# Kernel tuning notes

Hardware: AMD Instinct MI355X
Metric: run time of the kernel (lower is better)

## Reference

```python
import jax, jax.numpy as jnp
import numpy as np

N = 100000
D_IN = 256
C = 4          # num_classes
D_C = 32       # output_dim // num_classes
E = 1600000    # nnz per class adjacency


def setup_inputs() -> dict:
    key = jax.random.key(0)
    k1, k2, k3, k4, k5 = jax.random.split(key, 5)
    x = jax.random.normal(k1, (N, D_IN), dtype=jnp.float32)
    # kernel (input_dim, output_dim) split along axis=1 into C chunks -> [D_IN, C, D_C]
    W = jax.random.normal(k2, (D_IN, C, D_C), dtype=jnp.float32) * (2.0 / D_IN) ** 0.5
    rows = jax.random.randint(k3, (C, E), 0, N, dtype=jnp.int64)
    cols = jax.random.randint(k4, (C, E), 0, N, dtype=jnp.int64)
    vals = jax.random.uniform(k5, (C, E), dtype=jnp.float32)
    return {"x": x, "W": W, "rows": rows, "cols": cols, "vals": vals}


def reference(x, W, rows, cols, vals):
    # dropout with rate 0.0 is identity.
    n = x.shape[0]
    # per-class dense transform: tmp[:, c, :] = x @ W[:, c, :]
    tmp = jnp.einsum('nd,dcf->ncf', x, W)  # [N, C, D_C]

    def prop(r, c, v, t):
        # t: [N, D_C] features for one class; SpMM A_c @ t via gather+segment_sum
        msg = t[c] * v[:, None]                              # [E, D_C]
        return jax.ops.segment_sum(msg, r, num_segments=n)   # [N, D_C]

    out = jax.vmap(prop, in_axes=(0, 0, 0, 1))(rows, cols, vals, tmp)  # [C, N, D_C]
    z = jnp.transpose(out, (1, 0, 2)).reshape(n, -1)  # concat along feature axis -> [N, C*D_C]
    return jax.nn.relu(z)
```

## Files before the change

### kernel.cpp

```cpp
#include <hip/hip_runtime.h>
#include <hip/hip_bf16.h>
#include <hip/hip_fp16.h>

#define D_IN 256
#define D_OUT 128
#define D_C 32
#define NUM_C 4
#define RB_LOG 10
#define RB 1024
#define MB_MAX 400

typedef _Float16 f16x8 __attribute__((ext_vector_type(8)));
typedef float    f32x4 __attribute__((ext_vector_type(4)));

__global__ void wcvt_kernel(const float* __restrict__ W, __half* __restrict__ Wt) {
    int t = blockIdx.x * 256 + threadIdx.x;
    if (t >= D_IN * D_OUT) return;
    int col = t >> 8;
    int k   = t & 255;
    Wt[col * D_IN + k] = __float2half(W[k * D_OUT + col]);
}

__global__ __launch_bounds__(256) void gemm_kernel(const float* __restrict__ x,
                                                   const __half* __restrict__ Wt,
                                                   __half* __restrict__ tmp,
                                                   int Nrows) {
    __shared__ f16x8 As[2048];
    const int t    = threadIdx.x;
    const int brow = blockIdx.x * 64;

    const int w   = t >> 6;
    const int l   = t & 63;
    const int l15 = l & 15;
    const int hi  = l >> 4;

    f16x8 bf[8][2];
    #pragma unroll
    for (int ks = 0; ks < 8; ++ks)
        #pragma unroll
        for (int cti = 0; cti < 2; ++cti)
            bf[ks][cti] = *reinterpret_cast<const f16x8*>(
                Wt + (size_t)((w * 2 + cti) * 16 + l15) * D_IN + ks * 32 + hi * 8);

    #pragma unroll
    for (int i = 0; i < 8; ++i) {
        int ci  = i * 256 + t;
        int row = ci >> 5;
        int kc  = ci & 31;
        int grow = brow + row;
        float4 a0 = make_float4(0.f, 0.f, 0.f, 0.f);
        float4 a1 = make_float4(0.f, 0.f, 0.f, 0.f);
        if (grow < Nrows) {
            const float* src = x + (size_t)grow * D_IN + kc * 8;
            a0 = *reinterpret_cast<const float4*>(src);
            a1 = *reinterpret_cast<const float4*>(src + 4);
        }
        f16x8 h;
        h[0] = (_Float16)a0.x; h[1] = (_Float16)a0.y;
        h[2] = (_Float16)a0.z; h[3] = (_Float16)a0.w;
        h[4] = (_Float16)a1.x; h[5] = (_Float16)a1.y;
        h[6] = (_Float16)a1.z; h[7] = (_Float16)a1.w;
        As[kc * 64 + (row ^ kc)] = h;
    }
    __syncthreads();

    f32x4 acc[4][2] = {};

    #pragma unroll
    for (int rt = 0; rt < 4; ++rt) {
        const int arow = rt * 16 + l15;
        #pragma unroll
        for (int ks = 0; ks < 8; ++ks) {
            const int kcA = ks * 4 + hi;
            f16x8 afrag = As[kcA * 64 + (arow ^ kcA)];
            acc[rt][0] = __builtin_amdgcn_mfma_f32_16x16x32_f16(afrag, bf[ks][0], acc[rt][0], 0, 0, 0);
            acc[rt][1] = __builtin_amdgcn_mfma_f32_16x16x32_f16(afrag, bf[ks][1], acc[rt][1], 0, 0, 0);
        }
    }

    #pragma unroll
    for (int rt = 0; rt < 4; ++rt) {
        #pragma unroll
        for (int cti = 0; cti < 2; ++cti) {
            const int cio = cti * 16 + l15;
            #pragma unroll
            for (int r = 0; r < 4; ++r) {
                int grow = brow + rt * 16 + hi * 4 + r;
                if (grow < Nrows)
                    tmp[((size_t)w * Nrows + grow) * 32 + cio] = __float2half((float)acc[rt][cti][r]);
            }
        }
    }
}

__global__ __launch_bounds__(256) void bucket_hist_kernel(const int* __restrict__ rows,
                                                          int* __restrict__ bcnt,
                                                          int CE, int E, int NB, int MB) {
    __shared__ int h[MB_MAX];
    for (int i = threadIdx.x; i < MB; i += 256) h[i] = 0;
    __syncthreads();
    const int CE4 = CE >> 2;
    const int4* rows4 = reinterpret_cast<const int4*>(rows);
    int base4 = blockIdx.x * 4096;
    #pragma unroll 4
    for (int i = 0; i < 16; ++i) {
        int i4 = base4 + threadIdx.x + i * 256;
        if (i4 < CE4) {
            int e0 = i4 << 2;
            int c = (e0 >= 3 * E) ? 3 : (e0 >= 2 * E) ? 2 : (e0 >= E) ? 1 : 0;
            int4 rv = rows4[i4];
            atomicAdd(&h[c * NB + (rv.x >> RB_LOG)], 1);
            atomicAdd(&h[c * NB + (rv.y >> RB_LOG)], 1);
            atomicAdd(&h[c * NB + (rv.z >> RB_LOG)], 1);
            atomicAdd(&h[c * NB + (rv.w >> RB_LOG)], 1);
        }
    }
    if (blockIdx.x == 0 && threadIdx.x < (CE & 3)) {
        int e = (CE4 << 2) + threadIdx.x;
        int c = (e >= 3 * E) ? 3 : (e >= 2 * E) ? 2 : (e >= E) ? 1 : 0;
        atomicAdd(&h[c * NB + (rows[e] >> RB_LOG)], 1);
    }
    __syncthreads();
    for (int i = threadIdx.x; i < MB; i += 256)
        if (h[i]) atomicAdd(&bcnt[i], h[i]);
}

__global__ __launch_bounds__(512) void bucket_scan_kernel(const int* __restrict__ bcnt,
                                                          int* __restrict__ bstartP,
                                                          int* __restrict__ bheadLine,
                                                          int* __restrict__ bstartD,
                                                          int* __restrict__ starts,
                                                          int MB, int M, int slackLines) {
    __shared__ int sd[512];
    int t = threadIdx.x;
    int v = (t < MB) ? bcnt[t] : 0;
    int capL = ((v + 7) >> 3) + slackLines;
    sd[t] = capL; __syncthreads();
    for (int off = 1; off < 512; off <<= 1) {
        int add = (t >= off) ? sd[t - off] : 0;
        __syncthreads();
        sd[t] += add;
        __syncthreads();
    }
    int exclL = sd[t] - capL;
    if (t < MB) { bstartP[t] = exclL * 8; bheadLine[t] = exclL; }
    __syncthreads();
    sd[t] = v; __syncthreads();
    for (int off = 1; off < 512; off <<= 1) {
        int add = (t >= off) ? sd[t - off] : 0;
        __syncthreads();
        sd[t] += add;
        __syncthreads();
    }
    int exclD = sd[t] - v;
    if (t < MB) bstartD[t] = exclD;
    if (t == 511) starts[M] = sd[511];
}

__global__ __launch_bounds__(512) void partition_kernel(const int* __restrict__ rows,
                                                        const int* __restrict__ cols,
                                                        const float* __restrict__ vals,
                                                        int* __restrict__ bheadLine,
                                                        int2* __restrict__ arena,
                                                        int CE, int E, int NB, int MB) {
    __shared__ int lcnt[MB_MAX];
    __shared__ int lbase[MB_MAX];
    for (int i = threadIdx.x; i < MB; i += 512) lcnt[i] = 0;
    __syncthreads();
    int base = blockIdx.x * 8192;
    unsigned packed[16];
    #pragma unroll
    for (int i = 0; i < 16; ++i) {
        int e = base + threadIdx.x + i * 512;
        unsigned pk = 511u;
        if (e < CE) {
            int c = (e >= 3 * E) ? 3 : (e >= 2 * E) ? 2 : (e >= E) ? 1 : 0;
            int r = rows[e];
            int b = c * NB + (r >> RB_LOG);
            int rank = atomicAdd(&lcnt[b], 1);
            pk = (unsigned)b | ((unsigned)rank << 9) | ((unsigned)(r & (RB - 1)) << 22);
        }
        packed[i] = pk;
    }
    __syncthreads();
    for (int b = threadIdx.x; b < MB; b += 512) {
        int n = lcnt[b];
        lbase[b] = n ? atomicAdd(&bheadLine[b], (n + 7) >> 3) : 0;
    }
    __syncthreads();
    #pragma unroll
    for (int i = 0; i < 16; ++i) {
        unsigned pk = packed[i];
        int b = pk & 511u;
        if (b != 511) {
            int e    = base + threadIdx.x + i * 512;
            int rank = (pk >> 9) & 8191u;
            int rl   = pk >> 22;
            arena[lbase[b] * 8 + rank] = make_int2(cols[e] | (rl << 17), __float_as_int(vals[e]));
        }
    }
    for (int b = threadIdx.x; b < MB; b += 512) {
        int n = lcnt[b];
        if (n) {
            int end = ((n + 7) >> 3) * 8;
            for (int s = n; s < end; ++s)
                arena[lbase[b] * 8 + s] = make_int2(-1, 0);
        }
    }
}

__global__ __launch_bounds__(1024) void rowsort_kernel(const int* __restrict__ bstartP,
                                                       const int* __restrict__ bheadLine,
                                                       const int* __restrict__ bstartD,
                                                       const int2* __restrict__ src,
                                                       unsigned* __restrict__ dst,
                                                       int* __restrict__ starts,
                                                       int N, int NB) {
    __shared__ int lcnt[RB];
    __shared__ int sd[RB];
    int b = blockIdx.x;
    int c = b / NB, rb = b - c * NB;
    int t = threadIdx.x;
    int s = bstartP[b];
    int nspan = bheadLine[b] * 8 - s;
    int dbase = bstartD[b];

    lcnt[t] = 0;
    __syncthreads();
    for (int i = t; i < nspan; i += 1024) {
        unsigned u = (unsigned)src[s + i].x;
        if ((u & 0x1FFFFu) != 0x1FFFFu)
            atomicAdd(&lcnt[(u >> 17) & (RB - 1)], 1);
    }
    __syncthreads();
    int v = lcnt[t];
    sd[t] = v; __syncthreads();
    for (int off = 1; off < 1024; off <<= 1) {
        int add = (t >= off) ? sd[t - off] : 0;
        __syncthreads();
        sd[t] += add;
        __syncthreads();
    }
    int excl = sd[t] - v;
    int grow = (rb << RB_LOG) + t;
    if (grow < N) starts[c * N + grow] = dbase + excl;
    __syncthreads();
    lcnt[t] = excl;
    __syncthreads();
    for (int i = t; i < nspan; i += 1024) {
        int2 rec = src[s + i];
        unsigned u = (unsigned)rec.x;
        if ((u & 0x1FFFFu) != 0x1FFFFu) {
            int rl  = (u >> 17) & (RB - 1);
            int pos = atomicAdd(&lcnt[rl], 1);
            __half h = __float2half(__int_as_float(rec.y));
            unsigned hb = (unsigned)*reinterpret_cast<unsigned short*>(&h);
            dst[dbase + pos] = (hb << 17) | (u & 0x1FFFFu);
        }
    }
}

__global__ __launch_bounds__(256) void pull2_kernel(const int* __restrict__ starts,
                                                    const unsigned* __restrict__ arena,
                                                    const __half2* __restrict__ tmp2,
                                                    float* __restrict__ out,
                                                    int N, int M) {
    int p = blockIdx.x * 16 + (threadIdx.x >> 4);
    if (p >= M) return;
    const int lf = threadIdx.x & 15;
    int c   = p / N;
    int row = p - c * N;
    int s = starts[p];
    int n = starts[p + 1] - s;
    const __half2* tc = tmp2 + (size_t)c * N * 16 + lf;

    float2 acc = make_float2(0.f, 0.f);
    int base = 0;
    for (; base + 16 <= n; base += 16) {
        unsigned r[16];
        #pragma unroll
        for (int j = 0; j < 16; ++j) r[j] = arena[s + base + j];
        #pragma unroll
        for (int j = 0; j < 16; ++j) {
            unsigned short hb = (unsigned short)(r[j] >> 17);
            float v = __half2float(*reinterpret_cast<__half*>(&hb));
            float2 tv = __half22float2(tc[(size_t)(r[j] & 0x1FFFFu) * 16]);
            acc.x = fmaf(v, tv.x, acc.x);
            acc.y = fmaf(v, tv.y, acc.y);
        }
    }
    if (base + 8 <= n) {
        unsigned r[8];
        #pragma unroll
        for (int j = 0; j < 8; ++j) r[j] = arena[s + base + j];
        #pragma unroll
        for (int j = 0; j < 8; ++j) {
            unsigned short hb = (unsigned short)(r[j] >> 17);
            float v = __half2float(*reinterpret_cast<__half*>(&hb));
            float2 tv = __half22float2(tc[(size_t)(r[j] & 0x1FFFFu) * 16]);
            acc.x = fmaf(v, tv.x, acc.x);
            acc.y = fmaf(v, tv.y, acc.y);
        }
        base += 8;
    }
    for (; base < n; ++base) {
        unsigned u = arena[s + base];
        unsigned short hb = (unsigned short)(u >> 17);
        float v = __half2float(*reinterpret_cast<__half*>(&hb));
        float2 tv = __half22float2(tc[(size_t)(u & 0x1FFFFu) * 16]);
        acc.x = fmaf(v, tv.x, acc.x);
        acc.y = fmaf(v, tv.y, acc.y);
    }
    *reinterpret_cast<float2*>(&out[(size_t)row * D_OUT + c * D_C + 2 * lf]) =
        make_float2(fmaxf(acc.x, 0.f), fmaxf(acc.y, 0.f));
}

__global__ __launch_bounds__(256) void scatter_kernel(const int* __restrict__ rows,
                                                      const int* __restrict__ cols,
                                                      const float* __restrict__ vals,
                                                      const __half* __restrict__ tmp,
                                                      float* __restrict__ out,
                                                      long long totalEdges, int E, int N) {
    long long gid = (long long)blockIdx.x * 8 + (threadIdx.x >> 5);
    if (gid >= totalEdges) return;
    const int lane = threadIdx.x & 31;
    const long long e1 = E, e2 = 2LL * E, e3 = 3LL * E;
    int c = (gid >= e3) ? 3 : (gid >= e2) ? 2 : (gid >= e1) ? 1 : 0;
    const float tv = __half2float(tmp[((size_t)c * N + cols[gid]) * 32 + lane]);
    atomicAdd(&out[(size_t)rows[gid] * D_OUT + c * D_C + lane], tv * vals[gid]);
}

__global__ void relu_kernel(float* __restrict__ out, int n4) {
    int i = blockIdx.x * blockDim.x + threadIdx.x;
    if (i < n4) {
        float4 v = reinterpret_cast<float4*>(out)[i];
        v.x = fmaxf(v.x, 0.f); v.y = fmaxf(v.y, 0.f);
        v.z = fmaxf(v.z, 0.f); v.w = fmaxf(v.w, 0.f);
        reinterpret_cast<float4*>(out)[i] = v;
    }
}

extern "C" void kernel_launch(void* const* d_in, const int* in_sizes, int n_in,
                              void* d_out, int out_size, void* d_ws, size_t ws_size,
                              hipStream_t stream) {
    const float* x    = (const float*)d_in[0];
    const float* W    = (const float*)d_in[1];
    const int*   rows = (const int*)d_in[2];
    const int*   cols = (const int*)d_in[3];
    const float* vals = (const float*)d_in[4];
    float* out = (float*)d_out;

    const int N  = in_sizes[0] / D_IN;
    const int CE = in_sizes[2];
    const int E  = CE / NUM_C;
    const int NB = (N + RB - 1) >> RB_LOG;
    const int MB = NUM_C * NB;
    const int M  = NUM_C * N;

    const int partBlocks = (CE + 8191) / 8192;
    const int slackLines = (7 * partBlocks + 7) / 8 + 1;
    const long long capRecs = (long long)((CE + 7) & ~7) + (long long)MB * slackLines * 8 + (long long)MB * 8;

    size_t off = 0;
    __half* tmp  = (__half*)((char*)d_ws + off); off += (size_t)N * D_OUT * 2;
    off = (off + 15) & ~(size_t)15;
    __half* Wt   = (__half*)((char*)d_ws + off); off += (size_t)D_IN * D_OUT * 2;
    int* bcnt    = (int*)((char*)d_ws + off);   off += (size_t)MB * 4;
    int* bstartP = (int*)((char*)d_ws + off);   off += (size_t)MB * 4;
    int* bheadL  = (int*)((char*)d_ws + off);   off += (size_t)MB * 4;
    int* bstartD = (int*)((char*)d_ws + off);   off += (size_t)MB * 4;
    int* starts  = (int*)((char*)d_ws + off);   off += (size_t)(M + 1) * 4;
    off = (off + 63) & ~(size_t)63;
    int2* arena  = (int2*)((char*)d_ws + off);  off += (size_t)capRecs * 8;
    unsigned* sorted = (unsigned*)((char*)d_ws + off); off += (size_t)CE * 4;
    const bool ok = (off <= ws_size) && (MB <= MB_MAX) && (MB <= 512);

    wcvt_kernel<<<(D_IN * D_OUT + 255) / 256, 256, 0, stream>>>(W, Wt);
    const int gemmBlocks = (N + 63) / 64;
    gemm_kernel<<<gemmBlocks, 256, 0, stream>>>(x, Wt, tmp, N);

    if (ok) {
        hipMemsetAsync(bcnt, 0, (size_t)MB * 4, stream);
        const int histBlocks = ((CE >> 2) + 4095) / 4096;
        bucket_hist_kernel<<<histBlocks, 256, 0, stream>>>(rows, bcnt, CE, E, NB, MB);
        bucket_scan_kernel<<<1, 512, 0, stream>>>(bcnt, bstartP, bheadL, bstartD, starts, MB, M, slackLines);
        partition_kernel<<<partBlocks, 512, 0, stream>>>(rows, cols, vals, bheadL, arena, CE, E, NB, MB);
        rowsort_kernel<<<MB, 1024, 0, stream>>>(bstartP, bheadL, bstartD, arena, sorted, starts, N, NB);
        const int pullBlocks = (M + 15) / 16;
        pull2_kernel<<<pullBlocks, 256, 0, stream>>>(starts, sorted,
                                                     reinterpret_cast<const __half2*>(tmp), out, N, M);
    } else {
        hipMemsetAsync(d_out, 0, (size_t)out_size * sizeof(float), stream);
        const int scatterBlocks = (CE + 7) / 8;
        scatter_kernel<<<scatterBlocks, 256, 0, stream>>>(rows, cols, vals, tmp, out, (long long)CE, E, N);
        const int n4 = out_size / 4;
        relu_kernel<<<(n4 + 255) / 256, 256, 0, stream>>>(out, n4);
    }
}
```

Baseline: 312.8 us.

## Fuse GEMM with bucket histogram in one launch and widen pull gathers

Merges the dense GEMM and the row-bucket histogram into a single kernel whose grid is split by block index, so the two independent stages run concurrently and one launch is removed. Separately, the pull SpMM now gives each output row 8 lanes that each load 4 halves (8 bytes) instead of 16 lanes loading 2 halves, which halves the number of gather instructions per edge and writes float4 outputs. The fused kernel statically reserves LDS for both paths, which may lower occupancy. In the fallback path the histogram now runs and its memset is issued even when it is not needed.

```diff
diff --git a/kernel.cpp b/kernel.cpp
--- a/kernel.cpp
+++ b/kernel.cpp
@@ -21,108 +21,109 @@
     Wt[col * D_IN + k] = __float2half(W[k * D_OUT + col]);
 }
 
-__global__ __launch_bounds__(256) void gemm_kernel(const float* __restrict__ x,
-                                                   const __half* __restrict__ Wt,
-                                                   __half* __restrict__ tmp,
-                                                   int Nrows) {
+__global__ __launch_bounds__(256) void gemm_hist_kernel(const float* __restrict__ x,
+                                                        const __half* __restrict__ Wt,
+                                                        __half* __restrict__ tmp,
+                                                        int Nrows,
+                                                        const int* __restrict__ rows,
+                                                        int* __restrict__ bcnt,
+                                                        int CE, int E, int NB, int MB,
+                                                        int gemmBlocks) {
     __shared__ f16x8 As[2048];
-    const int t    = threadIdx.x;
-    const int brow = blockIdx.x * 64;
-
-    const int w   = t >> 6;
-    const int l   = t & 63;
-    const int l15 = l & 15;
-    const int hi  = l >> 4;
-
-    f16x8 bf[8][2];
-    #pragma unroll
-    for (int ks = 0; ks < 8; ++ks)
-        #pragma unroll
-        for (int cti = 0; cti < 2; ++cti)
-            bf[ks][cti] = *reinterpret_cast<const f16x8*>(
-                Wt + (size_t)((w * 2 + cti) * 16 + l15) * D_IN + ks * 32 + hi * 8);
-
-    #pragma unroll
-    for (int i = 0; i < 8; ++i) {
-        int ci  = i * 256 + t;
-        int row = ci >> 5;
-        int kc  = ci & 31;
-        int grow = brow + row;
-        float4 a0 = make_float4(0.f, 0.f, 0.f, 0.f);
-        float4 a1 = make_float4(0.f, 0.f, 0.f, 0.f);
-        if (grow < Nrows) {
-            const float* src = x + (size_t)grow * D_IN + kc * 8;
-            a0 = *reinterpret_cast<const float4*>(src);
-            a1 = *reinterpret_cast<const float4*>(src + 4);
-        }
-        f16x8 h;
-        h[0] = (_Float16)a0.x; h[1] = (_Float16)a0.y;
-        h[2] = (_Float16)a0.z; h[3] = (_Float16)a0.w;
-        h[4] = (_Float16)a1.x; h[5] = (_Float16)a1.y;
-        h[6] = (_Float16)a1.z; h[7] = (_Float16)a1.w;
-        As[kc * 64 + (row ^ kc)] = h;
-    }
-    __syncthreads();
-
-    f32x4 acc[4][2] = {};
-
-    #pragma unroll
-    for (int rt = 0; rt < 4; ++rt) {
-        const int arow = rt * 16 + l15;
-        #pragma unroll
-        for (int ks = 0; ks < 8; ++ks) {
-            const int kcA = ks * 4 + hi;
-            f16x8 afrag = As[kcA * 64 + (arow ^ kcA)];
-            acc[rt][0] = __builtin_amdgcn_mfma_f32_16x16x32_f16(afrag, bf[ks][0], acc[rt][0], 0, 0, 0);
-            acc[rt][1] = __builtin_amdgcn_mfma_f32_16x16x32_f16(afrag, bf[ks][1], acc[rt][1], 0, 0, 0);
-        }
-    }
-
-    #pragma unroll
-    for (int rt = 0; rt < 4; ++rt) {
-        #pragma unroll
-        for (int cti = 0; cti < 2; ++cti) {
-            const int cio = cti * 16 + l15;
+    __shared__ int   h[MB_MAX];
+    const int t = threadIdx.x;
+
+    if (blockIdx.x < gemmBlocks) {
+        const int brow = blockIdx.x * 64;
+        const int w   = t >> 6;
+        const int l   = t & 63;
+        const int l15 = l & 15;
+        const int hi  = l >> 4;
+
+        f16x8 bf[8][2];
+        #pragma unroll
+        for (int ks = 0; ks < 8; ++ks)
             #pragma unroll
-            for (int r = 0; r < 4; ++r) {
-                int grow = brow + rt * 16 + hi * 4 + r;
-                if (grow < Nrows)
-                    tmp[((size_t)w * Nrows + grow) * 32 + cio] = __float2half((float)acc[rt][cti][r]);
+            for (int cti = 0; cti < 2; ++cti)
+                bf[ks][cti] = *reinterpret_cast<const f16x8*>(
+                    Wt + (size_t)((w * 2 + cti) * 16 + l15) * D_IN + ks * 32 + hi * 8);
+
+        #pragma unroll
+        for (int i = 0; i < 8; ++i) {
+            int ci  = i * 256 + t;
+            int row = ci >> 5;
+            int kc  = ci & 31;
+            int grow = brow + row;
+            float4 a0 = make_float4(0.f, 0.f, 0.f, 0.f);
+            float4 a1 = make_float4(0.f, 0.f, 0.f, 0.f);
+            if (grow < Nrows) {
+                const float* src = x + (size_t)grow * D_IN + kc * 8;
+                a0 = *reinterpret_cast<const float4*>(src);
+                a1 = *reinterpret_cast<const float4*>(src + 4);
             }
-        }
-    }
-}
-
-__global__ __launch_bounds__(256) void bucket_hist_kernel(const int* __restrict__ rows,
-                                                          int* __restrict__ bcnt,
-                                                          int CE, int E, int NB, int MB) {
-    __shared__ int h[MB_MAX];
-    for (int i = threadIdx.x; i < MB; i += 256) h[i] = 0;
-    __syncthreads();
-    const int CE4 = CE >> 2;
-    const int4* rows4 = reinterpret_cast<const int4*>(rows);
-    int base4 = blockIdx.x * 4096;
-    #pragma unroll 4
-    for (int i = 0; i < 16; ++i) {
-        int i4 = base4 + threadIdx.x + i * 256;
-        if (i4 < CE4) {
-            int e0 = i4 << 2;
-            int c = (e0 >= 3 * E) ? 3 : (e0 >= 2 * E) ? 2 : (e0 >= E) ? 1 : 0;
-            int4 rv = rows4[i4];
-            atomicAdd(&h[c * NB + (rv.x >> RB_LOG)], 1);
-            atomicAdd(&h[c * NB + (rv.y >> RB_LOG)], 1);
-            atomicAdd(&h[c * NB + (rv.z >> RB_LOG)], 1);
-            atomicAdd(&h[c * NB + (rv.w >> RB_LOG)], 1);
-        }
-    }
-    if (blockIdx.x == 0 && threadIdx.x < (CE & 3)) {
-        int e = (CE4 << 2) + threadIdx.x;
-        int c = (e >= 3 * E) ? 3 : (e >= 2 * E) ? 2 : (e >= E) ? 1 : 0;
-        atomicAdd(&h[c * NB + (rows[e] >> RB_LOG)], 1);
-    }
-    __syncthreads();
-    for (int i = threadIdx.x; i < MB; i += 256)
-        if (h[i]) atomicAdd(&bcnt[i], h[i]);
+            f16x8 hh;
+            hh[0] = (_Float16)a0.x; hh[1] = (_Float16)a0.y;
+            hh[2] = (_Float16)a0.z; hh[3] = (_Float16)a0.w;
+            hh[4] = (_Float16)a1.x; hh[5] = (_Float16)a1.y;
+            hh[6] = (_Float16)a1.z; hh[7] = (_Float16)a1.w;
+            As[kc * 64 + (row ^ kc)] = hh;
+        }
+        __syncthreads();
+
+        f32x4 acc[4][2] = {};
+        #pragma unroll
+        for (int rt = 0; rt < 4; ++rt) {
+            const int arow = rt * 16 + l15;
+            #pragma unroll
+            for (int ks = 0; ks < 8; ++ks) {
+                const int kcA = ks * 4 + hi;
+                f16x8 afrag = As[kcA * 64 + (arow ^ kcA)];
+                acc[rt][0] = __builtin_amdgcn_mfma_f32_16x16x32_f16(afrag, bf[ks][0], acc[rt][0], 0, 0, 0);
+                acc[rt][1] = __builtin_amdgcn_mfma_f32_16x16x32_f16(afrag, bf[ks][1], acc[rt][1], 0, 0, 0);
+            }
+        }
+
+        #pragma unroll
+        for (int rt = 0; rt < 4; ++rt)
+            #pragma unroll
+            for (int cti = 0; cti < 2; ++cti) {
+                const int cio = cti * 16 + l15;
+                #pragma unroll
+                for (int r = 0; r < 4; ++r) {
+                    int grow = brow + rt * 16 + hi * 4 + r;
+                    if (grow < Nrows)
+                        tmp[((size_t)w * Nrows + grow) * 32 + cio] = __float2half((float)acc[rt][cti][r]);
+                }
+            }
+    } else {
+        const int bid = blockIdx.x - gemmBlocks;
+        for (int i = t; i < MB; i += 256) h[i] = 0;
+        __syncthreads();
+        const int CE4 = CE >> 2;
+        const int4* rows4 = reinterpret_cast<const int4*>(rows);
+        int base4 = bid * 4096;
+        #pragma unroll 4
+        for (int i = 0; i < 16; ++i) {
+            int i4 = base4 + t + i * 256;
+            if (i4 < CE4) {
+                int e0 = i4 << 2;
+                int c = (e0 >= 3 * E) ? 3 : (e0 >= 2 * E) ? 2 : (e0 >= E) ? 1 : 0;
+                int4 rv = rows4[i4];
+                atomicAdd(&h[c * NB + (rv.x >> RB_LOG)], 1);
+                atomicAdd(&h[c * NB + (rv.y >> RB_LOG)], 1);
+                atomicAdd(&h[c * NB + (rv.z >> RB_LOG)], 1);
+                atomicAdd(&h[c * NB + (rv.w >> RB_LOG)], 1);
+            }
+        }
+        if (bid == 0 && t < (CE & 3)) {
+            int e = (CE4 << 2) + t;
+            int c = (e >= 3 * E) ? 3 : (e >= 2 * E) ? 2 : (e >= E) ? 1 : 0;
+            atomicAdd(&h[c * NB + (rows[e] >> RB_LOG)], 1);
+        }
+        __syncthreads();
+        for (int i = t; i < MB; i += 256)
+            if (h[i]) atomicAdd(&bcnt[i], h[i]);
+    }
 }
 
 __global__ __launch_bounds__(512) void bucket_scan_kernel(const int* __restrict__ bcnt,
@@ -262,19 +263,19 @@
 
 __global__ __launch_bounds__(256) void pull2_kernel(const int* __restrict__ starts,
                                                     const unsigned* __restrict__ arena,
-                                                    const __half2* __restrict__ tmp2,
+                                                    const uint2* __restrict__ tmp4,
                                                     float* __restrict__ out,
                                                     int N, int M) {
-    int p = blockIdx.x * 16 + (threadIdx.x >> 4);
+    int p = blockIdx.x * 32 + (threadIdx.x >> 3);
     if (p >= M) return;
-    const int lf = threadIdx.x & 15;
+    const int lf = threadIdx.x & 7;
     int c   = p / N;
     int row = p - c * N;
     int s = starts[p];
     int n = starts[p + 1] - s;
-    const __half2* tc = tmp2 + (size_t)c * N * 16 + lf;
-
-    float2 acc = make_float2(0.f, 0.f);
+    const uint2* tc = tmp4 + (size_t)c * N * 8 + lf;
+
+    float4 acc = make_float4(0.f, 0.f, 0.f, 0.f);
     int base = 0;
     for (; base + 16 <= n; base += 16) {
         unsigned r[16];
@@ -284,9 +285,13 @@
         for (int j = 0; j < 16; ++j) {
             unsigned short hb = (unsigned short)(r[j] >> 17);
             float v = __half2float(*reinterpret_cast<__half*>(&hb));
-            float2 tv = __half22float2(tc[(size_t)(r[j] & 0x1FFFFu) * 16]);
-            acc.x = fmaf(v, tv.x, acc.x);
-            acc.y = fmaf(v, tv.y, acc.y);
+            uint2 tw = tc[(size_t)(r[j] & 0x1FFFFu) * 8];
+            float2 t0 = __half22float2(*reinterpret_cast<__half2*>(&tw.x));
+            float2 t1 = __half22float2(*reinterpret_cast<__half2*>(&tw.y));
+            acc.x = fmaf(v, t0.x, acc.x);
+            acc.y = fmaf(v, t0.y, acc.y);
+            acc.z = fmaf(v, t1.x, acc.z);
+            acc.w = fmaf(v, t1.y, acc.w);
         }
     }
     if (base + 8 <= n) {
@@ -297,9 +302,13 @@
         for (int j = 0; j < 8; ++j) {
             unsigned short hb = (unsigned short)(r[j] >> 17);
             float v = __half2float(*reinterpret_cast<__half*>(&hb));
-            float2 tv = __half22float2(tc[(size_t)(r[j] & 0x1FFFFu) * 16]);
-            acc.x = fmaf(v, tv.x, acc.x);
-            acc.y = fmaf(v, tv.y, acc.y);
+            uint2 tw = tc[(size_t)(r[j] & 0x1FFFFu) * 8];
+            float2 t0 = __half22float2(*reinterpret_cast<__half2*>(&tw.x));
+            float2 t1 = __half22float2(*reinterpret_cast<__half2*>(&tw.y));
+            acc.x = fmaf(v, t0.x, acc.x);
+            acc.y = fmaf(v, t0.y, acc.y);
+            acc.z = fmaf(v, t1.x, acc.z);
+            acc.w = fmaf(v, t1.y, acc.w);
         }
         base += 8;
     }
@@ -307,12 +316,17 @@
         unsigned u = arena[s + base];
         unsigned short hb = (unsigned short)(u >> 17);
         float v = __half2float(*reinterpret_cast<__half*>(&hb));
-        float2 tv = __half22float2(tc[(size_t)(u & 0x1FFFFu) * 16]);
-        acc.x = fmaf(v, tv.x, acc.x);
-        acc.y = fmaf(v, tv.y, acc.y);
-    }
-    *reinterpret_cast<float2*>(&out[(size_t)row * D_OUT + c * D_C + 2 * lf]) =
-        make_float2(fmaxf(acc.x, 0.f), fmaxf(acc.y, 0.f));
+        uint2 tw = tc[(size_t)(u & 0x1FFFFu) * 8];
+        float2 t0 = __half22float2(*reinterpret_cast<__half2*>(&tw.x));
+        float2 t1 = __half22float2(*reinterpret_cast<__half2*>(&tw.y));
+        acc.x = fmaf(v, t0.x, acc.x);
+        acc.y = fmaf(v, t0.y, acc.y);
+        acc.z = fmaf(v, t1.x, acc.z);
+        acc.w = fmaf(v, t1.y, acc.w);
+    }
+    *reinterpret_cast<float4*>(&out[(size_t)row * D_OUT + c * D_C + 4 * lf]) =
+        make_float4(fmaxf(acc.x, 0.f), fmaxf(acc.y, 0.f),
+                    fmaxf(acc.z, 0.f), fmaxf(acc.w, 0.f));
 }
 
 __global__ __launch_bounds__(256) void scatter_kernel(const int* __restrict__ rows,
@@ -376,19 +390,20 @@
     const bool ok = (off <= ws_size) && (MB <= MB_MAX) && (MB <= 512);
 
     wcvt_kernel<<<(D_IN * D_OUT + 255) / 256, 256, 0, stream>>>(W, Wt);
+
     const int gemmBlocks = (N + 63) / 64;
-    gemm_kernel<<<gemmBlocks, 256, 0, stream>>>(x, Wt, tmp, N);
+    const int histBlocks = ((CE >> 2) + 4095) / 4096;
+    hipMemsetAsync(bcnt, 0, (size_t)MB * 4, stream);
+    gemm_hist_kernel<<<gemmBlocks + histBlocks, 256, 0, stream>>>(
+        x, Wt, tmp, N, rows, bcnt, CE, E, NB, MB, gemmBlocks);
 
     if (ok) {
-        hipMemsetAsync(bcnt, 0, (size_t)MB * 4, stream);
-        const int histBlocks = ((CE >> 2) + 4095) / 4096;
-        bucket_hist_kernel<<<histBlocks, 256, 0, stream>>>(rows, bcnt, CE, E, NB, MB);
         bucket_scan_kernel<<<1, 512, 0, stream>>>(bcnt, bstartP, bheadL, bstartD, starts, MB, M, slackLines);
         partition_kernel<<<partBlocks, 512, 0, stream>>>(rows, cols, vals, bheadL, arena, CE, E, NB, MB);
         rowsort_kernel<<<MB, 1024, 0, stream>>>(bstartP, bheadL, bstartD, arena, sorted, starts, N, NB);
-        const int pullBlocks = (M + 15) / 16;
+        const int pullBlocks = (M + 31) / 32;
         pull2_kernel<<<pullBlocks, 256, 0, stream>>>(starts, sorted,
-                                                     reinterpret_cast<const __half2*>(tmp), out, N, M);
+                                                     reinterpret_cast<const uint2*>(tmp), out, N, M);
     } else {
         hipMemsetAsync(d_out, 0, (size_t)out_size * sizeof(float), stream);
         const int scatterBlocks = (CE + 7) / 8;
```

After: 294.5 us. 5.9% less time.
